# Optimization experiments

Measured on AMD Instinct MI355X. Metric: run time of the kernel, lower is better.

The kernel has to match this reference:

```python
import jax, jax.numpy as jnp
import numpy as np

N_EMBD = 126
N_HEADS = 6
HEAD_DIM = N_EMBD // N_HEADS  # 21


def setup_inputs() -> dict:
    key = jax.random.key(0)
    k1, k2, k3 = jax.random.split(key, 3)
    B, T = 8, 2048
    x = jax.random.normal(k1, (B, T, N_EMBD), dtype=jnp.float32)
    # torch Linear weights stored as (out, in); we store transposed (in, out) for x @ W
    w_attn = jax.random.normal(k2, (N_EMBD, 3 * N_EMBD), dtype=jnp.float32) * (1.0 / np.sqrt(N_EMBD))
    w_proj = jax.random.normal(k3, (N_EMBD, N_EMBD), dtype=jnp.float32) * (1.0 / np.sqrt(N_EMBD))
    return {"x": x, "w_attn": w_attn, "w_proj": w_proj}


def reference(x, w_attn, w_proj):
    B, T, C = x.shape
    qkv = x @ w_attn                      # [B, T, 3C]
    q, k, v = jnp.split(qkv, 3, axis=-1)  # each [B, T, C]

    def heads(t):  # [B,T,C] -> [B,H,T,hd]
        return t.reshape(B, T, N_HEADS, HEAD_DIM).transpose(0, 2, 1, 3)

    q, k, v = heads(q), heads(k), heads(v)
    scale = 1.0 / np.sqrt(HEAD_DIM).astype(np.float32)
    scores = jnp.einsum('bhqd,bhkd->bhqk', q, k) * scale  # [B,H,T,T]
    causal = jnp.tril(jnp.ones((T, T), dtype=bool))
    scores = jnp.where(causal, scores, jnp.finfo(scores.dtype).min)
    attn = jax.nn.softmax(scores, axis=-1)
    out = jnp.einsum('bhqk,bhkd->bhqd', attn, v)           # [B,H,T,hd]
    out = out.transpose(0, 2, 1, 3).reshape(B, T, C)
    return out @ w_proj
```

## Files before the change

kernel.cpp:

```cpp
#include <hip/hip_runtime.h>
#include <hip/hip_bf16.h>


#define B_ 8
#define T_ 2048
#define C_ 126
#define H_ 6
#define D_ 21
#define TC_ 378
#define KP_ 128
#define DP_ 32
#define M_ 16384
#define QSCALE 0.31481923469333463f

typedef __hip_bfloat16 bf16;
typedef __bf16 bf16_t;
typedef __bf16 bf16x2 __attribute__((ext_vector_type(2)));
typedef __bf16 bf16x8 __attribute__((ext_vector_type(8)));
typedef float f32x4 __attribute__((ext_vector_type(4)));
typedef int int2v __attribute__((ext_vector_type(2)));

__device__ __forceinline__ float ldf(const bf16* p, long i) { return __bfloat162float(p[i]); }
__device__ __forceinline__ float ldf(const float* p, long i) { return p[i]; }
__device__ __forceinline__ void stf(bf16* p, long i, float v) { p[i] = __float2bfloat16(v); }
__device__ __forceinline__ void stf(float* p, long i, float v) { p[i] = v; }

__device__ __forceinline__ float fexp2(float x) {
#if __has_builtin(__builtin_amdgcn_exp2f)
  return __builtin_amdgcn_exp2f(x);
#else
  float r; asm("v_exp_f32 %0, %1" : "=v"(r) : "v"(x)); return r;
#endif
}

__device__ __forceinline__ unsigned int ld2(const bf16* x, long i) {
  return *(const unsigned int*)((const unsigned short*)x + i);
}
__device__ __forceinline__ unsigned int ld2(const float* x, long i) {
  const float2 f = *(const float2*)(x + i);
  union { bf16_t b[2]; unsigned int u; } cv;
  cv.b[0] = (bf16_t)f.x; cv.b[1] = (bf16_t)f.y;
  return cv.u;
}

__device__ __forceinline__ void probe_dtype(const void* x, int tid, int* sflag) {
  if (tid < 64) {
    const unsigned int w = ((const unsigned int*)x)[tid * 97 + 13];
    const unsigned int e = (w >> 7) & 0xFF;
    const bool bflike = (e >= 115 && e <= 131) || ((w & 0x7FFFu) == 0);
    const unsigned long long mask = __ballot(bflike);
    if (tid == 0) *sflag = (__popcll(mask) >= 40) ? 1 : 0;
  }
  __syncthreads();
}

template <typename T>
__device__ __forceinline__ void prep_w_body(const T* __restrict__ wa,
                                            const T* __restrict__ wp,
                                            bf16_t* __restrict__ WTa,
                                            bf16_t* __restrict__ WTp) {
  const int stride = gridDim.x * blockDim.x;
  const int idx0 = blockIdx.x * blockDim.x + threadIdx.x;
  for (int i = idx0; i < 384 * KP_ + KP_ * KP_; i += stride) {
    if (i < 384 * KP_) {
      const int n = i >> 7, k = i & 127;
      WTa[i] = (k < C_ && n < TC_) ? (bf16_t)ldf(wa, (long)k * TC_ + n) : (bf16_t)0.f;
    } else {
      const int j = i - 384 * KP_;
      const int n = j >> 7, k = j & 127;
      WTp[j] = (k < C_ && n < C_) ? (bf16_t)ldf(wp, (long)k * C_ + n) : (bf16_t)0.f;
    }
  }
}

__global__ __launch_bounds__(256) void prep_w_kernel(
    const void* __restrict__ x, const void* __restrict__ wa,
    const void* __restrict__ wp, bf16_t* __restrict__ WTa,
    bf16_t* __restrict__ WTp) {
  __shared__ int sflag;
  probe_dtype(x, threadIdx.x, &sflag);
  if (sflag) prep_w_body<bf16>((const bf16*)wa, (const bf16*)wp, WTa, WTp);
  else       prep_w_body<float>((const float*)wa, (const float*)wp, WTa, WTp);
}

#define QS_ 40

template <typename T>
__device__ __forceinline__ void qkv_body(
    const T* __restrict__ x, const bf16_t* __restrict__ WT,
    bf16_t* __restrict__ Qb, bf16_t* __restrict__ Kb, bf16_t* __restrict__ VT,
    bf16_t* __restrict__ xs, bf16_t* __restrict__ qbuf,
    bf16_t* __restrict__ kbuf, bf16_t* __restrict__ vbuf) {
  const int m0 = blockIdx.x * 32;
  const int tid = threadIdx.x;
  for (int i = tid; i < 32 * 64; i += 256) {
    const int row = i >> 6, cp = i & 63;
    unsigned int v = 0;
    if (cp < 63) v = ld2(x, (long)(m0 + row) * C_ + 2 * cp);
    ((unsigned int*)xs)[i] = v;
  }
  for (int i = tid; i < 6 * 32 * 11; i += 256) {
    const int h = i / 352, rem = i - h * 352, t = rem / 11, d = 21 + rem % 11;
    qbuf[(h * 32 + t) * QS_ + d] = (bf16_t)0.f;
    kbuf[(h * 32 + t) * QS_ + d] = (bf16_t)0.f;
  }
  for (int i = tid; i < 6 * 11 * 32; i += 256) {
    const int h = i / 352, rem = i - h * 352, d = 21 + rem / 32, t = rem % 32;
    vbuf[(h * 32 + d) * 32 + t] = (d == 21) ? (bf16_t)1.f : (bf16_t)0.f;
  }
  __syncthreads();

  const int wv = tid >> 6, lane = tid & 63;
  const int lr = lane & 15, quad = lane >> 4;
  const bf16_t* arU = xs + lr * KP_ + quad * 8;
  const bf16_t* arL = xs + (16 + lr) * KP_ + quad * 8;
  const bf16x8 aU0 = *(const bf16x8*)(arU);
  const bf16x8 aU1 = *(const bf16x8*)(arU + 32);
  const bf16x8 aU2 = *(const bf16x8*)(arU + 64);
  const bf16x8 aU3 = *(const bf16x8*)(arU + 96);
  const bf16x8 aL0 = *(const bf16x8*)(arL);
  const bf16x8 aL1 = *(const bf16x8*)(arL + 32);
  const bf16x8 aL2 = *(const bf16x8*)(arL + 64);
  const bf16x8 aL3 = *(const bf16x8*)(arL + 96);

  for (int nt = wv; nt < 24; nt += 4) {
    const int n0 = nt * 16;
    const bf16x8* bp = (const bf16x8*)(WT + (long)(n0 + lr) * KP_ + quad * 8);
    const bf16x8 b0 = bp[0], b1 = bp[4], b2 = bp[8], b3 = bp[12];
    f32x4 accU = {0.f, 0.f, 0.f, 0.f};
    f32x4 accL = {0.f, 0.f, 0.f, 0.f};
    accU = __builtin_amdgcn_mfma_f32_16x16x32_bf16(aU0, b0, accU, 0, 0, 0);
    accU = __builtin_amdgcn_mfma_f32_16x16x32_bf16(aU1, b1, accU, 0, 0, 0);
    accU = __builtin_amdgcn_mfma_f32_16x16x32_bf16(aU2, b2, accU, 0, 0, 0);
    accU = __builtin_amdgcn_mfma_f32_16x16x32_bf16(aU3, b3, accU, 0, 0, 0);
    accL = __builtin_amdgcn_mfma_f32_16x16x32_bf16(aL0, b0, accL, 0, 0, 0);
    accL = __builtin_amdgcn_mfma_f32_16x16x32_bf16(aL1, b1, accL, 0, 0, 0);
    accL = __builtin_amdgcn_mfma_f32_16x16x32_bf16(aL2, b2, accL, 0, 0, 0);
    accL = __builtin_amdgcn_mfma_f32_16x16x32_bf16(aL3, b3, accL, 0, 0, 0);

    const int c = n0 + lr;
    if (c < TC_) {
      const int which = c / C_;
      const int cc = c - which * C_;
      const int h = cc / D_, d = cc - h * D_;
#pragma unroll
      for (int r = 0; r < 4; ++r) {
        const int tU = quad * 4 + r;
        const int tL = 16 + tU;
        if (which == 0) {
          qbuf[(h * 32 + tU) * QS_ + d] = (bf16_t)(accU[r] * QSCALE);
          qbuf[(h * 32 + tL) * QS_ + d] = (bf16_t)(accL[r] * QSCALE);
        } else if (which == 1) {
          kbuf[(h * 32 + tU) * QS_ + d] = (bf16_t)accU[r];
          kbuf[(h * 32 + tL) * QS_ + d] = (bf16_t)accL[r];
        } else {
          vbuf[(h * 32 + d) * 32 + tU] = (bf16_t)accU[r];
          vbuf[(h * 32 + d) * 32 + tL] = (bf16_t)accL[r];
        }
      }
    }
  }
  __syncthreads();

  const int b = m0 >> 11, t0 = m0 & 2047;
  for (int i = tid; i < 384; i += 256) {
    const int j = (i < 192) ? i : i - 192;
    const int h = j >> 5, t = j & 31;
    const int4* src = (const int4*)(((i < 192) ? qbuf : kbuf) + (h * 32 + t) * QS_);
    int4* dst = (int4*)((((i < 192) ? Qb : Kb)) + ((long)(b * H_ + h) * T_ + (t0 + t)) * DP_);
    dst[0] = src[0]; dst[1] = src[1]; dst[2] = src[2]; dst[3] = src[3];
  }
  for (int i = tid; i < 192; i += 256) {
    const int h = i >> 5, d = i & 31;
    const int4* src = (const int4*)(vbuf + (h * 32 + d) * 32);
    int4* dst = (int4*)(VT + ((long)(b * H_ + h) * DP_ + d) * T_ + t0);
    dst[0] = src[0]; dst[1] = src[1]; dst[2] = src[2]; dst[3] = src[3];
  }
}

__global__ __launch_bounds__(256) void qkv_mfma(
    const void* __restrict__ x, const bf16_t* __restrict__ WT,
    bf16_t* __restrict__ Qb, bf16_t* __restrict__ Kb, bf16_t* __restrict__ VT) {
  __shared__ __align__(16) bf16_t xs[32 * KP_];
  __shared__ __align__(16) bf16_t qbuf[6 * 32 * QS_];
  __shared__ __align__(16) bf16_t kbuf[6 * 32 * QS_];
  __shared__ __align__(16) bf16_t vbuf[6 * 32 * 32];
  __shared__ int sflag;
  probe_dtype(x, threadIdx.x, &sflag);
  if (sflag) qkv_body<bf16>((const bf16*)x, WT, Qb, Kb, VT, xs, qbuf, kbuf, vbuf);
  else       qkv_body<float>((const float*)x, WT, Qb, Kb, VT, xs, qbuf, kbuf, vbuf);
}

__device__ __forceinline__ void swap32(int& a, int& b) {
#if __has_builtin(__builtin_amdgcn_permlane32_swap)
  const int2v r = __builtin_amdgcn_permlane32_swap(a, b, false, false);
  a = r[0]; b = r[1];
#else
  const int sa = __shfl_xor(a, 32, 64), sb = __shfl_xor(b, 32, 64);
  const bool hi = (threadIdx.x & 32) != 0;
  a = hi ? sb : a;
  b = hi ? b : sa;
#endif
}

__device__ __forceinline__ void swap16(int& a, int& b) {
#if __has_builtin(__builtin_amdgcn_permlane16_swap)
  const int2v r = __builtin_amdgcn_permlane16_swap(a, b, false, false);
  a = r[0]; b = r[1];
#else
  const int sa = __shfl_xor(a, 16, 64), sb = __shfl_xor(b, 16, 64);
  const bool odd = (threadIdx.x & 16) != 0;
  a = odd ? sb : a;
  b = odd ? b : sa;
#endif
}

__device__ __forceinline__ int pkbf(float x, float y) {
  union { bf16x2 h; int i; } u;
  u.h[0] = (bf16_t)x; u.h[1] = (bf16_t)y;
  return u.i;
}

__device__ __forceinline__ bf16x8 build_frag(const f32x4 g1, const f32x4 g2) {
  int a1 = pkbf(g1[0], g1[1]);
  int b1 = pkbf(g1[2], g1[3]);
  int a2 = pkbf(g2[0], g2[1]);
  int b2 = pkbf(g2[2], g2[3]);
  swap32(a1, a2); swap32(b1, b2);
  swap16(a1, a2); swap16(b1, b2);
  union { int i[4]; bf16x8 v; } u;
  u.i[0] = a1; u.i[1] = b1; u.i[2] = a2; u.i[3] = b2;
  return u.v;
}

__global__ __launch_bounds__(256, 2) void attn_mfma(
    const bf16_t* __restrict__ Qb, const bf16_t* __restrict__ Kb,
    const bf16_t* __restrict__ VT, bf16_t* __restrict__ ATTp) {
  __shared__ __align__(16) float smem[4352];
  const int bh = blockIdx.x;
  const int qb = 31 - blockIdx.y;
  const int d0 = 2 * qb, d1 = d0 + 1;
  const int q0 = qb * 64;
  const int tid = threadIdx.x;
  const int wv = tid >> 6, lane = tid & 63;
  const int lr = lane & 15, quad = lane >> 4;
  const int mq = quad * 4;

  const bf16_t* Qbh = Qb + (long)bh * T_ * DP_;
  const bf16_t* Kbh = Kb + (long)bh * T_ * DP_;
  const bf16_t* VTbh = VT + (long)bh * DP_ * T_;

  const bf16x8 qA0 = *(const bf16x8*)(Qbh + (long)(q0 + lr) * DP_ + quad * 8);
  const bf16x8 qA1 = *(const bf16x8*)(Qbh + (long)(q0 + 16 + lr) * DP_ + quad * 8);
  const bf16x8 qB0 = *(const bf16x8*)(Qbh + (long)(q0 + 32 + lr) * DP_ + quad * 8);
  const bf16x8 qB1 = *(const bf16x8*)(Qbh + (long)(q0 + 48 + lr) * DP_ + quad * 8);

  f32x4 oA00 = {0.f,0.f,0.f,0.f}, oA01 = {0.f,0.f,0.f,0.f};
  f32x4 oA10 = {0.f,0.f,0.f,0.f}, oA11 = {0.f,0.f,0.f,0.f};
  f32x4 oB00 = {0.f,0.f,0.f,0.f}, oB01 = {0.f,0.f,0.f,0.f};
  f32x4 oB10 = {0.f,0.f,0.f,0.f}, oB11 = {0.f,0.f,0.f,0.f};

  for (int t = wv; t <= d1; t += 4) {
    const int kb = t * 32;
    const bool do0 = (t <= d0);
    const bf16x8 k0 = *(const bf16x8*)(Kbh + (long)(kb + lr) * DP_ + quad * 8);
    const bf16x8 k1 = *(const bf16x8*)(Kbh + (long)(kb + 16 + lr) * DP_ + quad * 8);

    f32x4 sA00 = {0.f,0.f,0.f,0.f}, sA01 = {0.f,0.f,0.f,0.f};
    f32x4 sA10 = {0.f,0.f,0.f,0.f}, sA11 = {0.f,0.f,0.f,0.f};
    f32x4 sB00 = {0.f,0.f,0.f,0.f}, sB01 = {0.f,0.f,0.f,0.f};
    f32x4 sB10 = {0.f,0.f,0.f,0.f}, sB11 = {0.f,0.f,0.f,0.f};
    __builtin_amdgcn_s_setprio(1);
    if (do0) {
      sA00 = __builtin_amdgcn_mfma_f32_16x16x32_bf16(k0, qA0, sA00, 0, 0, 0);
      sA01 = __builtin_amdgcn_mfma_f32_16x16x32_bf16(k0, qA1, sA01, 0, 0, 0);
      sA10 = __builtin_amdgcn_mfma_f32_16x16x32_bf16(k1, qA0, sA10, 0, 0, 0);
      sA11 = __builtin_amdgcn_mfma_f32_16x16x32_bf16(k1, qA1, sA11, 0, 0, 0);
    }
    sB00 = __builtin_amdgcn_mfma_f32_16x16x32_bf16(k0, qB0, sB00, 0, 0, 0);
    sB01 = __builtin_amdgcn_mfma_f32_16x16x32_bf16(k0, qB1, sB01, 0, 0, 0);
    sB10 = __builtin_amdgcn_mfma_f32_16x16x32_bf16(k1, qB0, sB10, 0, 0, 0);
    sB11 = __builtin_amdgcn_mfma_f32_16x16x32_bf16(k1, qB1, sB11, 0, 0, 0);
    __builtin_amdgcn_s_setprio(0);

    const bf16x8 v0 = *(const bf16x8*)(VTbh + (long)lr * T_ + kb + quad * 8);
    const bf16x8 v1 = *(const bf16x8*)(VTbh + (long)(16 + lr) * T_ + kb + quad * 8);

    if (t == d0) {
#pragma unroll
      for (int r = 0; r < 4; ++r) {
        if (mq + r > lr) { sA00[r] = -1e30f; sA11[r] = -1e30f; }
        sA10[r] = -1e30f;
      }
    }
    if (t == d1) {
#pragma unroll
      for (int r = 0; r < 4; ++r) {
        if (mq + r > lr) { sB00[r] = -1e30f; sB11[r] = -1e30f; }
        sB10[r] = -1e30f;
      }
    }
    if (do0) {
#pragma unroll
      for (int r = 0; r < 4; ++r) {
        sA00[r] = fexp2(sA00[r]); sA01[r] = fexp2(sA01[r]);
        sA10[r] = fexp2(sA10[r]); sA11[r] = fexp2(sA11[r]);
      }
    }
#pragma unroll
    for (int r = 0; r < 4; ++r) {
      sB00[r] = fexp2(sB00[r]); sB01[r] = fexp2(sB01[r]);
      sB10[r] = fexp2(sB10[r]); sB11[r] = fexp2(sB11[r]);
    }

    __builtin_amdgcn_s_setprio(1);
    if (do0) {
      const bf16x8 pA0 = build_frag(sA00, sA10);
      const bf16x8 pA1 = build_frag(sA01, sA11);
      oA00 = __builtin_amdgcn_mfma_f32_16x16x32_bf16(pA0, v0, oA00, 0, 0, 0);
      oA01 = __builtin_amdgcn_mfma_f32_16x16x32_bf16(pA0, v1, oA01, 0, 0, 0);
      oA10 = __builtin_amdgcn_mfma_f32_16x16x32_bf16(pA1, v0, oA10, 0, 0, 0);
      oA11 = __builtin_amdgcn_mfma_f32_16x16x32_bf16(pA1, v1, oA11, 0, 0, 0);
    }
    {
      const bf16x8 pB0 = build_frag(sB00, sB10);
      const bf16x8 pB1 = build_frag(sB01, sB11);
      oB00 = __builtin_amdgcn_mfma_f32_16x16x32_bf16(pB0, v0, oB00, 0, 0, 0);
      oB01 = __builtin_amdgcn_mfma_f32_16x16x32_bf16(pB0, v1, oB01, 0, 0, 0);
      oB10 = __builtin_amdgcn_mfma_f32_16x16x32_bf16(pB1, v0, oB10, 0, 0, 0);
      oB11 = __builtin_amdgcn_mfma_f32_16x16x32_bf16(pB1, v1, oB11, 0, 0, 0);
    }
    __builtin_amdgcn_s_setprio(0);
  }

  const int b = bh / H_, h = bh - b * H_;

  __syncthreads();
  {
    float* my = smem + (wv * 64 + lane) * 17;
#pragma unroll
    for (int j = 0; j < 4; ++j) {
      my[j]      = oA00[j];
      my[4 + j]  = oA01[j];
      my[8 + j]  = oA10[j];
      my[12 + j] = oA11[j];
    }
  }
  __syncthreads();
  if (wv == 0) {
    float tot[16];
#pragma unroll
    for (int j = 0; j < 16; ++j)
      tot[j] = smem[lane * 17 + j] + smem[(64 + lane) * 17 + j] +
               smem[(128 + lane) * 17 + j] + smem[(192 + lane) * 17 + j];
#pragma unroll
    for (int r = 0; r < 4; ++r) {
      const float rl0 = 1.f / __shfl(tot[4 + r],  (lane & 48) + 5, 64);
      const float rl1 = 1.f / __shfl(tot[12 + r], (lane & 48) + 5, 64);
      const int qA = q0 + mq + r, qB2 = qA + 16;
      bf16_t* opA = ATTp + (long)(b * T_ + qA) * KP_ + h * D_;
      bf16_t* opB = ATTp + (long)(b * T_ + qB2) * KP_ + h * D_;
      opA[lr] = (bf16_t)(tot[r] * rl0);
      opB[lr] = (bf16_t)(tot[8 + r] * rl1);
      if (lr < 5) {
        opA[16 + lr] = (bf16_t)(tot[4 + r] * rl0);
        opB[16 + lr] = (bf16_t)(tot[12 + r] * rl1);
      }
    }
  }

  __syncthreads();
  {
    float* my = smem + (wv * 64 + lane) * 17;
#pragma unroll
    for (int j = 0; j < 4; ++j) {
      my[j]      = oB00[j];
      my[4 + j]  = oB01[j];
      my[8 + j]  = oB10[j];
      my[12 + j] = oB11[j];
    }
  }
  __syncthreads();
  if (wv == 0) {
    float tot[16];
#pragma unroll
    for (int j = 0; j < 16; ++j)
      tot[j] = smem[lane * 17 + j] + smem[(64 + lane) * 17 + j] +
               smem[(128 + lane) * 17 + j] + smem[(192 + lane) * 17 + j];
#pragma unroll
    for (int r = 0; r < 4; ++r) {
      const float rl0 = 1.f / __shfl(tot[4 + r],  (lane & 48) + 5, 64);
      const float rl1 = 1.f / __shfl(tot[12 + r], (lane & 48) + 5, 64);
      const int qA = q0 + 32 + mq + r, qB2 = qA + 16;
      bf16_t* opA = ATTp + (long)(b * T_ + qA) * KP_ + h * D_;
      bf16_t* opB = ATTp + (long)(b * T_ + qB2) * KP_ + h * D_;
      opA[lr] = (bf16_t)(tot[r] * rl0);
      opB[lr] = (bf16_t)(tot[8 + r] * rl1);
      if (lr < 5) {
        opA[16 + lr] = (bf16_t)(tot[4 + r] * rl0);
        opB[16 + lr] = (bf16_t)(tot[12 + r] * rl1);
      }
    }
  }
}

__global__ __launch_bounds__(256) void proj_mfma(
    const void* __restrict__ x, const bf16_t* __restrict__ ATTp,
    const bf16_t* __restrict__ WT, void* __restrict__ out) {
  __shared__ int sflag;
  probe_dtype(x, threadIdx.x, &sflag);
  const int isbf = sflag;

  const int m0 = blockIdx.x * 32;
  const int tid = threadIdx.x;
  const int wv = tid >> 6, lane = tid & 63;
  const int lr = lane & 15, quad = lane >> 4;

  const bf16x8* apU = (const bf16x8*)(ATTp + (long)(m0 + lr) * KP_ + quad * 8);
  const bf16x8* apL = (const bf16x8*)(ATTp + (long)(m0 + 16 + lr) * KP_ + quad * 8);
  const bf16x8 aU0 = apU[0], aU1 = apU[4], aU2 = apU[8], aU3 = apU[12];
  const bf16x8 aL0 = apL[0], aL1 = apL[4], aL2 = apL[8], aL3 = apL[12];

  for (int nt = wv; nt < 8; nt += 4) {
    const int n0 = nt * 16;
    const bf16x8* bp = (const bf16x8*)(WT + (long)(n0 + lr) * KP_ + quad * 8);
    const bf16x8 b0 = bp[0], b1 = bp[4], b2 = bp[8], b3 = bp[12];
    f32x4 accU = {0.f, 0.f, 0.f, 0.f};
    f32x4 accL = {0.f, 0.f, 0.f, 0.f};
    accU = __builtin_amdgcn_mfma_f32_16x16x32_bf16(aU0, b0, accU, 0, 0, 0);
    accU = __builtin_amdgcn_mfma_f32_16x16x32_bf16(aU1, b1, accU, 0, 0, 0);
    accU = __builtin_amdgcn_mfma_f32_16x16x32_bf16(aU2, b2, accU, 0, 0, 0);
    accU = __builtin_amdgcn_mfma_f32_16x16x32_bf16(aU3, b3, accU, 0, 0, 0);
    accL = __builtin_amdgcn_mfma_f32_16x16x32_bf16(aL0, b0, accL, 0, 0, 0);
    accL = __builtin_amdgcn_mfma_f32_16x16x32_bf16(aL1, b1, accL, 0, 0, 0);
    accL = __builtin_amdgcn_mfma_f32_16x16x32_bf16(aL2, b2, accL, 0, 0, 0);
    accL = __builtin_amdgcn_mfma_f32_16x16x32_bf16(aL3, b3, accL, 0, 0, 0);

    const int c = n0 + lr;
    if (c < C_) {
#pragma unroll
      for (int r = 0; r < 4; ++r) {
        const int mU = m0 + quad * 4 + r;
        const int mL = mU + 16;
        if (isbf) {
          stf((bf16*)out,  (long)mU * C_ + c, accU[r]);
          stf((bf16*)out,  (long)mL * C_ + c, accL[r]);
        } else {
          stf((float*)out, (long)mU * C_ + c, accU[r]);
          stf((float*)out, (long)mL * C_ + c, accL[r]);
        }
      }
    }
  }
}

extern "C" void kernel_launch(void* const* d_in, const int* in_sizes, int n_in,
                              void* d_out, int out_size, void* d_ws, size_t ws_size,
                              hipStream_t stream) {
  const void* x      = d_in[0];
  const void* w_attn = d_in[1];
  const void* w_proj = d_in[2];

  char* base = (char*)d_ws;
  const long QKV = (long)48 * T_ * DP_;
  bf16_t* Qb = (bf16_t*)(base + 256);
  bf16_t* Kb = Qb + QKV;
  bf16_t* VT = Kb + QKV;
  bf16_t* WTa  = VT + QKV;
  bf16_t* WTp  = WTa + 384 * KP_;
  bf16_t* ATTp = WTp + KP_ * KP_;

  prep_w_kernel<<<64, 256, 0, stream>>>(x, w_attn, w_proj, WTa, WTp);
  qkv_mfma<<<M_ / 32, 256, 0, stream>>>(x, WTa, Qb, Kb, VT);
  attn_mfma<<<dim3(48, 32), 256, 0, stream>>>(Qb, Kb, VT, ATTp);
  proj_mfma<<<M_ / 32, 256, 0, stream>>>(x, ATTp, WTp, d_out);
}
```

Before: 116.7 us.

## Double attention query tile to 128 rows per block to reuse K/V loads

Each attention block now handles 128 query rows (four 32-row groups) instead of 64, so every K and V fragment loaded is reused across twice as many queries. The grid is halved to 48x16 and launch bounds relaxed to one block per SIMD set, since register use grows with the extra accumulators. The aim is to cut global K/V traffic and per-block overhead. The cost is lower occupancy, fewer blocks for load balancing across the causal triangle, and a longer serial merge of the four output groups.

```diff
diff --git a/kernel.cpp b/kernel.cpp
--- a/kernel.cpp
+++ b/kernel.cpp
@@ -233,14 +233,31 @@
   return u.v;
 }
 
-__global__ __launch_bounds__(256, 2) void attn_mfma(
+__device__ __forceinline__ void diag_mask(f32x4& s00, f32x4& s10, f32x4& s11,
+                                          int mq, int lr) {
+#pragma unroll
+  for (int r = 0; r < 4; ++r) {
+    if (mq + r > lr) { s00[r] = -1e30f; s11[r] = -1e30f; }
+    s10[r] = -1e30f;
+  }
+}
+
+__device__ __forceinline__ void exp4(f32x4& a, f32x4& b, f32x4& c, f32x4& d) {
+#pragma unroll
+  for (int r = 0; r < 4; ++r) {
+    a[r] = fexp2(a[r]); b[r] = fexp2(b[r]);
+    c[r] = fexp2(c[r]); d[r] = fexp2(d[r]);
+  }
+}
+
+__global__ __launch_bounds__(256, 1) void attn_mfma(
     const bf16_t* __restrict__ Qb, const bf16_t* __restrict__ Kb,
     const bf16_t* __restrict__ VT, bf16_t* __restrict__ ATTp) {
   __shared__ __align__(16) float smem[4352];
   const int bh = blockIdx.x;
-  const int qb = 31 - blockIdx.y;
-  const int d0 = 2 * qb, d1 = d0 + 1;
-  const int q0 = qb * 64;
+  const int qb = 15 - blockIdx.y;
+  const int d0 = 4 * qb, d1 = d0 + 1, d2 = d0 + 2, d3 = d0 + 3;
+  const int q0 = qb * 128;
   const int tid = threadIdx.x;
   const int wv = tid >> 6, lane = tid & 63;
   const int lr = lane & 15, quad = lane >> 4;
@@ -254,154 +271,156 @@
   const bf16x8 qA1 = *(const bf16x8*)(Qbh + (long)(q0 + 16 + lr) * DP_ + quad * 8);
   const bf16x8 qB0 = *(const bf16x8*)(Qbh + (long)(q0 + 32 + lr) * DP_ + quad * 8);
   const bf16x8 qB1 = *(const bf16x8*)(Qbh + (long)(q0 + 48 + lr) * DP_ + quad * 8);
+  const bf16x8 qC0 = *(const bf16x8*)(Qbh + (long)(q0 + 64 + lr) * DP_ + quad * 8);
+  const bf16x8 qC1 = *(const bf16x8*)(Qbh + (long)(q0 + 80 + lr) * DP_ + quad * 8);
+  const bf16x8 qD0 = *(const bf16x8*)(Qbh + (long)(q0 + 96 + lr) * DP_ + quad * 8);
+  const bf16x8 qD1 = *(const bf16x8*)(Qbh + (long)(q0 + 112 + lr) * DP_ + quad * 8);
 
   f32x4 oA00 = {0.f,0.f,0.f,0.f}, oA01 = {0.f,0.f,0.f,0.f};
   f32x4 oA10 = {0.f,0.f,0.f,0.f}, oA11 = {0.f,0.f,0.f,0.f};
   f32x4 oB00 = {0.f,0.f,0.f,0.f}, oB01 = {0.f,0.f,0.f,0.f};
   f32x4 oB10 = {0.f,0.f,0.f,0.f}, oB11 = {0.f,0.f,0.f,0.f};
-
-  for (int t = wv; t <= d1; t += 4) {
+  f32x4 oC00 = {0.f,0.f,0.f,0.f}, oC01 = {0.f,0.f,0.f,0.f};
+  f32x4 oC10 = {0.f,0.f,0.f,0.f}, oC11 = {0.f,0.f,0.f,0.f};
+  f32x4 oD00 = {0.f,0.f,0.f,0.f}, oD01 = {0.f,0.f,0.f,0.f};
+  f32x4 oD10 = {0.f,0.f,0.f,0.f}, oD11 = {0.f,0.f,0.f,0.f};
+
+  for (int t = wv; t <= d3; t += 4) {
     const int kb = t * 32;
-    const bool do0 = (t <= d0);
     const bf16x8 k0 = *(const bf16x8*)(Kbh + (long)(kb + lr) * DP_ + quad * 8);
     const bf16x8 k1 = *(const bf16x8*)(Kbh + (long)(kb + 16 + lr) * DP_ + quad * 8);
 
-    f32x4 sA00 = {0.f,0.f,0.f,0.f}, sA01 = {0.f,0.f,0.f,0.f};
-    f32x4 sA10 = {0.f,0.f,0.f,0.f}, sA11 = {0.f,0.f,0.f,0.f};
-    f32x4 sB00 = {0.f,0.f,0.f,0.f}, sB01 = {0.f,0.f,0.f,0.f};
-    f32x4 sB10 = {0.f,0.f,0.f,0.f}, sB11 = {0.f,0.f,0.f,0.f};
+    f32x4 sC00 = {0.f,0.f,0.f,0.f}, sC01 = {0.f,0.f,0.f,0.f};
+    f32x4 sC10 = {0.f,0.f,0.f,0.f}, sC11 = {0.f,0.f,0.f,0.f};
+    f32x4 sD00 = {0.f,0.f,0.f,0.f}, sD01 = {0.f,0.f,0.f,0.f};
+    f32x4 sD10 = {0.f,0.f,0.f,0.f}, sD11 = {0.f,0.f,0.f,0.f};
     __builtin_amdgcn_s_setprio(1);
-    if (do0) {
-      sA00 = __builtin_amdgcn_mfma_f32_16x16x32_bf16(k0, qA0, sA00, 0, 0, 0);
-      sA01 = __builtin_amdgcn_mfma_f32_16x16x32_bf16(k0, qA1, sA01, 0, 0, 0);
-      sA10 = __builtin_amdgcn_mfma_f32_16x16x32_bf16(k1, qA0, sA10, 0, 0, 0);
-      sA11 = __builtin_amdgcn_mfma_f32_16x16x32_bf16(k1, qA1, sA11, 0, 0, 0);
-    }
-    sB00 = __builtin_amdgcn_mfma_f32_16x16x32_bf16(k0, qB0, sB00, 0, 0, 0);
-    sB01 = __builtin_amdgcn_mfma_f32_16x16x32_bf16(k0, qB1, sB01, 0, 0, 0);
-    sB10 = __builtin_amdgcn_mfma_f32_16x16x32_bf16(k1, qB0, sB10, 0, 0, 0);
-    sB11 = __builtin_amdgcn_mfma_f32_16x16x32_bf16(k1, qB1, sB11, 0, 0, 0);
+    if (t <= d2) {
+      sC00 = __builtin_amdgcn_mfma_f32_16x16x32_bf16(k0, qC0, sC00, 0, 0, 0);
+      sC01 = __builtin_amdgcn_mfma_f32_16x16x32_bf16(k0, qC1, sC01, 0, 0, 0);
+      sC10 = __builtin_amdgcn_mfma_f32_16x16x32_bf16(k1, qC0, sC10, 0, 0, 0);
+      sC11 = __builtin_amdgcn_mfma_f32_16x16x32_bf16(k1, qC1, sC11, 0, 0, 0);
+    }
+    sD00 = __builtin_amdgcn_mfma_f32_16x16x32_bf16(k0, qD0, sD00, 0, 0, 0);
+    sD01 = __builtin_amdgcn_mfma_f32_16x16x32_bf16(k0, qD1, sD01, 0, 0, 0);
+    sD10 = __builtin_amdgcn_mfma_f32_16x16x32_bf16(k1, qD0, sD10, 0, 0, 0);
+    sD11 = __builtin_amdgcn_mfma_f32_16x16x32_bf16(k1, qD1, sD11, 0, 0, 0);
     __builtin_amdgcn_s_setprio(0);
 
     const bf16x8 v0 = *(const bf16x8*)(VTbh + (long)lr * T_ + kb + quad * 8);
     const bf16x8 v1 = *(const bf16x8*)(VTbh + (long)(16 + lr) * T_ + kb + quad * 8);
 
-    if (t == d0) {
+    if (t == d2) diag_mask(sC00, sC10, sC11, mq, lr);
+    if (t == d3) diag_mask(sD00, sD10, sD11, mq, lr);
+    if (t <= d2) exp4(sC00, sC01, sC10, sC11);
+    exp4(sD00, sD01, sD10, sD11);
+
+    __builtin_amdgcn_s_setprio(1);
+    if (t <= d2) {
+      const bf16x8 pC0 = build_frag(sC00, sC10);
+      const bf16x8 pC1 = build_frag(sC01, sC11);
+      oC00 = __builtin_amdgcn_mfma_f32_16x16x32_bf16(pC0, v0, oC00, 0, 0, 0);
+      oC01 = __builtin_amdgcn_mfma_f32_16x16x32_bf16(pC0, v1, oC01, 0, 0, 0);
+      oC10 = __builtin_amdgcn_mfma_f32_16x16x32_bf16(pC1, v0, oC10, 0, 0, 0);
+      oC11 = __builtin_amdgcn_mfma_f32_16x16x32_bf16(pC1, v1, oC11, 0, 0, 0);
+    }
+    {
+      const bf16x8 pD0 = build_frag(sD00, sD10);
+      const bf16x8 pD1 = build_frag(sD01, sD11);
+      oD00 = __builtin_amdgcn_mfma_f32_16x16x32_bf16(pD0, v0, oD00, 0, 0, 0);
+      oD01 = __builtin_amdgcn_mfma_f32_16x16x32_bf16(pD0, v1, oD01, 0, 0, 0);
+      oD10 = __builtin_amdgcn_mfma_f32_16x16x32_bf16(pD1, v0, oD10, 0, 0, 0);
+      oD11 = __builtin_amdgcn_mfma_f32_16x16x32_bf16(pD1, v1, oD11, 0, 0, 0);
+    }
+    __builtin_amdgcn_s_setprio(0);
+
+    if (t <= d1) {
+      f32x4 sA00 = {0.f,0.f,0.f,0.f}, sA01 = {0.f,0.f,0.f,0.f};
+      f32x4 sA10 = {0.f,0.f,0.f,0.f}, sA11 = {0.f,0.f,0.f,0.f};
+      f32x4 sB00 = {0.f,0.f,0.f,0.f}, sB01 = {0.f,0.f,0.f,0.f};
+      f32x4 sB10 = {0.f,0.f,0.f,0.f}, sB11 = {0.f,0.f,0.f,0.f};
+      __builtin_amdgcn_s_setprio(1);
+      if (t <= d0) {
+        sA00 = __builtin_amdgcn_mfma_f32_16x16x32_bf16(k0, qA0, sA00, 0, 0, 0);
+        sA01 = __builtin_amdgcn_mfma_f32_16x16x32_bf16(k0, qA1, sA01, 0, 0, 0);
+        sA10 = __builtin_amdgcn_mfma_f32_16x16x32_bf16(k1, qA0, sA10, 0, 0, 0);
+        sA11 = __builtin_amdgcn_mfma_f32_16x16x32_bf16(k1, qA1, sA11, 0, 0, 0);
+      }
+      sB00 = __builtin_amdgcn_mfma_f32_16x16x32_bf16(k0, qB0, sB00, 0, 0, 0);
+      sB01 = __builtin_amdgcn_mfma_f32_16x16x32_bf16(k0, qB1, sB01, 0, 0, 0);
+      sB10 = __builtin_amdgcn_mfma_f32_16x16x32_bf16(k1, qB0, sB10, 0, 0, 0);
+      sB11 = __builtin_amdgcn_mfma_f32_16x16x32_bf16(k1, qB1, sB11, 0, 0, 0);
+      __builtin_amdgcn_s_setprio(0);
+
+      if (t == d0) diag_mask(sA00, sA10, sA11, mq, lr);
+      if (t == d1) diag_mask(sB00, sB10, sB11, mq, lr);
+      if (t <= d0) exp4(sA00, sA01, sA10, sA11);
+      exp4(sB00, sB01, sB10, sB11);
+
+      __builtin_amdgcn_s_setprio(1);
+      if (t <= d0) {
+        const bf16x8 pA0 = build_frag(sA00, sA10);
+        const bf16x8 pA1 = build_frag(sA01, sA11);
+        oA00 = __builtin_amdgcn_mfma_f32_16x16x32_bf16(pA0, v0, oA00, 0, 0, 0);
+        oA01 = __builtin_amdgcn_mfma_f32_16x16x32_bf16(pA0, v1, oA01, 0, 0, 0);
+        oA10 = __builtin_amdgcn_mfma_f32_16x16x32_bf16(pA1, v0, oA10, 0, 0, 0);
+        oA11 = __builtin_amdgcn_mfma_f32_16x16x32_bf16(pA1, v1, oA11, 0, 0, 0);
+      }
+      {
+        const bf16x8 pB0 = build_frag(sB00, sB10);
+        const bf16x8 pB1 = build_frag(sB01, sB11);
+        oB00 = __builtin_amdgcn_mfma_f32_16x16x32_bf16(pB0, v0, oB00, 0, 0, 0);
+        oB01 = __builtin_amdgcn_mfma_f32_16x16x32_bf16(pB0, v1, oB01, 0, 0, 0);
+        oB10 = __builtin_amdgcn_mfma_f32_16x16x32_bf16(pB1, v0, oB10, 0, 0, 0);
+        oB11 = __builtin_amdgcn_mfma_f32_16x16x32_bf16(pB1, v1, oB11, 0, 0, 0);
+      }
+      __builtin_amdgcn_s_setprio(0);
+    }
+  }
+
+  const int b = bh / H_, h = bh - b * H_;
+
+  auto merge_pass = [&](const f32x4& m00, const f32x4& m01,
+                        const f32x4& m10, const f32x4& m11, int qoff) {
+    __syncthreads();
+    {
+      float* my = smem + (wv * 64 + lane) * 17;
+#pragma unroll
+      for (int j = 0; j < 4; ++j) {
+        my[j]      = m00[j];
+        my[4 + j]  = m01[j];
+        my[8 + j]  = m10[j];
+        my[12 + j] = m11[j];
+      }
+    }
+    __syncthreads();
+    if (wv == 0) {
+      float tot[16];
+#pragma unroll
+      for (int j = 0; j < 16; ++j)
+        tot[j] = smem[lane * 17 + j] + smem[(64 + lane) * 17 + j] +
+                 smem[(128 + lane) * 17 + j] + smem[(192 + lane) * 17 + j];
 #pragma unroll
       for (int r = 0; r < 4; ++r) {
-        if (mq + r > lr) { sA00[r] = -1e30f; sA11[r] = -1e30f; }
-        sA10[r] = -1e30f;
-      }
-    }
-    if (t == d1) {
-#pragma unroll
-      for (int r = 0; r < 4; ++r) {
-        if (mq + r > lr) { sB00[r] = -1e30f; sB11[r] = -1e30f; }
-        sB10[r] = -1e30f;
-      }
-    }
-    if (do0) {
-#pragma unroll
-      for (int r = 0; r < 4; ++r) {
-        sA00[r] = fexp2(sA00[r]); sA01[r] = fexp2(sA01[r]);
-        sA10[r] = fexp2(sA10[r]); sA11[r] = fexp2(sA11[r]);
-      }
-    }
-#pragma unroll
-    for (int r = 0; r < 4; ++r) {
-      sB00[r] = fexp2(sB00[r]); sB01[r] = fexp2(sB01[r]);
-      sB10[r] = fexp2(sB10[r]); sB11[r] = fexp2(sB11[r]);
-    }
-
-    __builtin_amdgcn_s_setprio(1);
-    if (do0) {
-      const bf16x8 pA0 = build_frag(sA00, sA10);
-      const bf16x8 pA1 = build_frag(sA01, sA11);
-      oA00 = __builtin_amdgcn_mfma_f32_16x16x32_bf16(pA0, v0, oA00, 0, 0, 0);
-      oA01 = __builtin_amdgcn_mfma_f32_16x16x32_bf16(pA0, v1, oA01, 0, 0, 0);
-      oA10 = __builtin_amdgcn_mfma_f32_16x16x32_bf16(pA1, v0, oA10, 0, 0, 0);
-      oA11 = __builtin_amdgcn_mfma_f32_16x16x32_bf16(pA1, v1, oA11, 0, 0, 0);
-    }
-    {
-      const bf16x8 pB0 = build_frag(sB00, sB10);
-      const bf16x8 pB1 = build_frag(sB01, sB11);
-      oB00 = __builtin_amdgcn_mfma_f32_16x16x32_bf16(pB0, v0, oB00, 0, 0, 0);
-      oB01 = __builtin_amdgcn_mfma_f32_16x16x32_bf16(pB0, v1, oB01, 0, 0, 0);
-      oB10 = __builtin_amdgcn_mfma_f32_16x16x32_bf16(pB1, v0, oB10, 0, 0, 0);
-      oB11 = __builtin_amdgcn_mfma_f32_16x16x32_bf16(pB1, v1, oB11, 0, 0, 0);
-    }
-    __builtin_amdgcn_s_setprio(0);
-  }
-
-  const int b = bh / H_, h = bh - b * H_;
-
-  __syncthreads();
-  {
-    float* my = smem + (wv * 64 + lane) * 17;
-#pragma unroll
-    for (int j = 0; j < 4; ++j) {
-      my[j]      = oA00[j];
-      my[4 + j]  = oA01[j];
-      my[8 + j]  = oA10[j];
-      my[12 + j] = oA11[j];
-    }
-  }
-  __syncthreads();
-  if (wv == 0) {
-    float tot[16];
-#pragma unroll
-    for (int j = 0; j < 16; ++j)
-      tot[j] = smem[lane * 17 + j] + smem[(64 + lane) * 17 + j] +
-               smem[(128 + lane) * 17 + j] + smem[(192 + lane) * 17 + j];
-#pragma unroll
-    for (int r = 0; r < 4; ++r) {
-      const float rl0 = 1.f / __shfl(tot[4 + r],  (lane & 48) + 5, 64);
-      const float rl1 = 1.f / __shfl(tot[12 + r], (lane & 48) + 5, 64);
-      const int qA = q0 + mq + r, qB2 = qA + 16;
-      bf16_t* opA = ATTp + (long)(b * T_ + qA) * KP_ + h * D_;
-      bf16_t* opB = ATTp + (long)(b * T_ + qB2) * KP_ + h * D_;
-      opA[lr] = (bf16_t)(tot[r] * rl0);
-      opB[lr] = (bf16_t)(tot[8 + r] * rl1);
-      if (lr < 5) {
-        opA[16 + lr] = (bf16_t)(tot[4 + r] * rl0);
-        opB[16 + lr] = (bf16_t)(tot[12 + r] * rl1);
-      }
-    }
-  }
-
-  __syncthreads();
-  {
-    float* my = smem + (wv * 64 + lane) * 17;
-#pragma unroll
-    for (int j = 0; j < 4; ++j) {
-      my[j]      = oB00[j];
-      my[4 + j]  = oB01[j];
-      my[8 + j]  = oB10[j];
-      my[12 + j] = oB11[j];
-    }
-  }
-  __syncthreads();
-  if (wv == 0) {
-    float tot[16];
-#pragma unroll
-    for (int j = 0; j < 16; ++j)
-      tot[j] = smem[lane * 17 + j] + smem[(64 + lane) * 17 + j] +
-               smem[(128 + lane) * 17 + j] + smem[(192 + lane) * 17 + j];
-#pragma unroll
-    for (int r = 0; r < 4; ++r) {
-      const float rl0 = 1.f / __shfl(tot[4 + r],  (lane & 48) + 5, 64);
-      const float rl1 = 1.f / __shfl(tot[12 + r], (lane & 48) + 5, 64);
-      const int qA = q0 + 32 + mq + r, qB2 = qA + 16;
-      bf16_t* opA = ATTp + (long)(b * T_ + qA) * KP_ + h * D_;
-      bf16_t* opB = ATTp + (long)(b * T_ + qB2) * KP_ + h * D_;
-      opA[lr] = (bf16_t)(tot[r] * rl0);
-      opB[lr] = (bf16_t)(tot[8 + r] * rl1);
-      if (lr < 5) {
-        opA[16 + lr] = (bf16_t)(tot[4 + r] * rl0);
-        opB[16 + lr] = (bf16_t)(tot[12 + r] * rl1);
-      }
-    }
-  }
+        const float rl0 = 1.f / __shfl(tot[4 + r],  (lane & 48) + 5, 64);
+        const float rl1 = 1.f / __shfl(tot[12 + r], (lane & 48) + 5, 64);
+        const int qA = q0 + qoff + mq + r, qB2 = qA + 16;
+        bf16_t* opA = ATTp + (long)(b * T_ + qA) * KP_ + h * D_;
+        bf16_t* opB = ATTp + (long)(b * T_ + qB2) * KP_ + h * D_;
+        opA[lr] = (bf16_t)(tot[r] * rl0);
+        opB[lr] = (bf16_t)(tot[8 + r] * rl1);
+        if (lr < 5) {
+          opA[16 + lr] = (bf16_t)(tot[4 + r] * rl0);
+          opB[16 + lr] = (bf16_t)(tot[12 + r] * rl1);
+        }
+      }
+    }
+  };
+
+  merge_pass(oA00, oA01, oA10, oA11, 0);
+  merge_pass(oB00, oB01, oB10, oB11, 32);
+  merge_pass(oC00, oC01, oC10, oC11, 64);
+  merge_pass(oD00, oD01, oD10, oD11, 96);
 }
 
 __global__ __launch_bounds__(256) void proj_mfma(
@@ -472,6 +491,6 @@
 
   prep_w_kernel<<<64, 256, 0, stream>>>(x, w_attn, w_proj, WTa, WTp);
   qkv_mfma<<<M_ / 32, 256, 0, stream>>>(x, WTa, Qb, Kb, VT);
-  attn_mfma<<<dim3(48, 32), 256, 0, stream>>>(Qb, Kb, VT, ATTp);
+  attn_mfma<<<dim3(48, 16), 256, 0, stream>>>(Qb, Kb, VT, ATTp);
   proj_mfma<<<M_ / 32, 256, 0, stream>>>(x, ATTp, WTp, d_out);
 }
```

Measured after the change: 131.9 us. 1.13x slower.
